# Kernel optimization log

Measured on AMD Instinct MI355X. Metric: run time of the kernel, lower is better.

The kernel has to match this reference:

```python
import jax, jax.numpy as jnp
import numpy as np

EPS = 1e-08


def _norm(H, add):
    # Faithful to GTN.norm: transpose, mask/set diagonal, row-normalize by degree, transpose back.
    # The original O(N^3) mm(deg_inv_diag, H) is expressed as an O(N^2) row scaling (same math).
    Ht = H.T
    n = Ht.shape[0]
    eye = jnp.eye(n, dtype=H.dtype)
    Ht = Ht * (1.0 - eye)
    if add:
        Ht = Ht + eye
    deg = jnp.sum(Ht, axis=1)
    deg_inv = jnp.where(deg == 0, 0.0, 1.0 / (deg + EPS))
    return (deg_inv[:, None] * Ht).T


def _gtconv(A, w):
    # A: [E, N, N]; w: [C, E, 1, 1] -> softmax over E, weighted sum of adjacency channels.
    s = jax.nn.softmax(w[:, :, 0, 0], axis=1)  # [C, E]
    return jnp.einsum('ce,eij->cij', s, A)     # [C, N, N]


def setup_inputs() -> dict:
    key = jax.random.key(0)
    k = jax.random.split(key, 6)
    E, N, C, w_in, w_out = 5, 2048, 2, 256, 64
    A = jax.random.uniform(k[0], (E, N, N), dtype=jnp.float32)
    X = jax.random.normal(k[1], (N, w_in), dtype=jnp.float32)
    conv_w_l0_1 = jax.random.normal(k[2], (C, E, 1, 1), dtype=jnp.float32)
    conv_w_l0_2 = jax.random.normal(k[3], (C, E, 1, 1), dtype=jnp.float32)
    conv_w_l1 = jax.random.normal(k[4], (C, E, 1, 1), dtype=jnp.float32)
    gcn_weight = jax.random.normal(k[5], (w_in, w_out), dtype=jnp.float32) * (1.0 / np.sqrt(w_in))
    return {"A": A, "X": X, "conv_w_l0_1": conv_w_l0_1, "conv_w_l0_2": conv_w_l0_2,
            "conv_w_l1": conv_w_l1, "gcn_weight": gcn_weight}


def reference(A, X, conv_w_l0_1, conv_w_l0_2, conv_w_l1, gcn_weight):
    N = A.shape[1]
    # Layer 0 (first=True): two GTConvs, meta-path composition via bmm.
    a = _gtconv(A, conv_w_l0_1)            # [C, N, N]
    b = _gtconv(A, conv_w_l0_2)            # [C, N, N]
    H = jnp.einsum('cij,cjk->cik', a, b)   # [C, N, N]
    # Layer 1 (first=False): normalize per channel, then compose with new conv.
    H = jax.vmap(lambda h: _norm(h, False))(H)
    a1 = _gtconv(A, conv_w_l1)
    H = jnp.einsum('cij,cjk->cik', H, a1)
    # GCN readout per channel: mm(norm_add(H_c).T, X @ W), relu, concat along features.
    Xw = X @ gcn_weight                     # [N, w_out]
    Hn = jax.vmap(lambda h: _norm(h, True))(H)   # [C, N, N]
    Xc = jax.nn.relu(jnp.einsum('cji,jk->cik', Hn, Xw))  # [C, N, w_out]
    X_ = jnp.transpose(Xc, (1, 0, 2)).reshape(N, -1)     # [N, C*w_out]
    return X_
```

## Files before the change

kernel.cpp:

```cpp
#include <hip/hip_runtime.h>
#include <cstdint>
#include <cstddef>

typedef unsigned short u16;
typedef __attribute__((ext_vector_type(8))) short short8;
typedef __attribute__((ext_vector_type(4))) float v4f;

static constexpr size_t NN = (size_t)2048 * 2048;
#define N2 2048

typedef __attribute__((address_space(1))) const unsigned int guint;
typedef __attribute__((address_space(3))) unsigned int luint;

__device__ __forceinline__ float b2f_bits(uint32_t hi) { union { uint32_t u; float f; } v; v.u = hi; return v.f; }
__device__ __forceinline__ float b2f(u16 x) { return b2f_bits((uint32_t)x << 16); }
__device__ __forceinline__ u16 f2b(float f) {
  union { float f; uint32_t u; } v; v.f = f;
  uint32_t r = v.u + 0x7fffu + ((v.u >> 16) & 1u);
  return (u16)(r >> 16);
}
__device__ __forceinline__ uint2 pack4(const float* f) {
  uint2 u;
  u.x = (uint32_t)f2b(f[0]) | ((uint32_t)f2b(f[1]) << 16);
  u.y = (uint32_t)f2b(f[2]) | ((uint32_t)f2b(f[3]) << 16);
  return u;
}
__device__ __forceinline__ uint4 pack8(const float* f) {
  uint4 u;
  u.x = (uint32_t)f2b(f[0]) | ((uint32_t)f2b(f[1]) << 16);
  u.y = (uint32_t)f2b(f[2]) | ((uint32_t)f2b(f[3]) << 16);
  u.z = (uint32_t)f2b(f[4]) | ((uint32_t)f2b(f[5]) << 16);
  u.w = (uint32_t)f2b(f[6]) | ((uint32_t)f2b(f[7]) << 16);
  return u;
}

__global__ __launch_bounds__(256, 6) void conv_kernel(
    const float* __restrict__ A, const float* __restrict__ w1,
    const float* __restrict__ w2, const float* __restrict__ w3,
    const float* __restrict__ X, const float* __restrict__ W,
    u16* __restrict__ abf, u16* __restrict__ bbt, u16* __restrict__ a1t,
    u16* __restrict__ Xwt)
{
  __shared__ float lb[32][33];
  __shared__ float la[32][33];
  const int t = threadIdx.x;
  const int i0 = blockIdx.y * 32, j0 = blockIdx.x * 32;

  float s1[2][5], s2[2][5], s3[2][5];
  {
    const float* wsrc[3] = { w1, w2, w3 };
    float (*sdst[3])[5] = { s1, s2, s3 };
    for (int q = 0; q < 3; ++q)
      for (int c = 0; c < 2; ++c) {
        float v[5], m = -1e30f, sum = 0.f;
        for (int e = 0; e < 5; ++e) { v[e] = wsrc[q][c * 5 + e]; m = fmaxf(m, v[e]); }
        for (int e = 0; e < 5; ++e) { v[e] = expf(v[e] - m); sum += v[e]; }
        for (int e = 0; e < 5; ++e) sdst[q][c][e] = v[e] / sum;
      }
  }

  const int row = t >> 3;
  const int c4 = (t & 7) * 4;
  float cst[2][4];

  {
    float fa[5][4];
    for (int e = 0; e < 5; ++e) {
      float4 v = *(const float4*)(A + (size_t)e * NN + (size_t)(i0 + row) * N2 + (j0 + c4));
      fa[e][0] = v.x; fa[e][1] = v.y; fa[e][2] = v.z; fa[e][3] = v.w;
    }
    for (int c = 0; c < 2; ++c) {
      float av[4] = {0,0,0,0}, bv[4] = {0,0,0,0}, cv[4] = {0,0,0,0};
      for (int e = 0; e < 5; ++e)
        #pragma unroll
        for (int u = 0; u < 4; ++u) {
          av[u] += s1[c][e] * fa[e][u];
          bv[u] += s2[c][e] * fa[e][u];
          cv[u] += s3[c][e] * fa[e][u];
        }
      *(uint2*)(abf + (size_t)c * NN + (size_t)(i0 + row) * N2 + (j0 + c4)) = pack4(av);
      float* ldst = (c == 0) ? &lb[row][c4] : &la[row][c4];
      #pragma unroll
      for (int u = 0; u < 4; ++u) ldst[u] = bv[u];
      #pragma unroll
      for (int u = 0; u < 4; ++u) cst[c][u] = cv[u];
    }
  }
  __syncthreads();
  {
    float t0[4], t1[4];
    #pragma unroll
    for (int u = 0; u < 4; ++u) { t0[u] = lb[c4 + u][row]; t1[u] = la[c4 + u][row]; }
    *(uint2*)(bbt + 0 * NN + (size_t)(j0 + row) * N2 + (i0 + c4)) = pack4(t0);
    *(uint2*)(bbt + 1 * NN + (size_t)(j0 + row) * N2 + (i0 + c4)) = pack4(t1);
  }
  __syncthreads();
  #pragma unroll
  for (int u = 0; u < 4; ++u) { lb[row][c4 + u] = cst[0][u]; la[row][c4 + u] = cst[1][u]; }
  __syncthreads();
  {
    float t0[4], t1[4];
    #pragma unroll
    for (int u = 0; u < 4; ++u) { t0[u] = lb[c4 + u][row]; t1[u] = la[c4 + u][row]; }
    *(uint2*)(a1t + 0 * NN + (size_t)(j0 + row) * N2 + (i0 + c4)) = pack4(t0);
    *(uint2*)(a1t + 1 * NN + (size_t)(j0 + row) * N2 + (i0 + c4)) = pack4(t1);
  }
  if (blockIdx.y < 8) {
    const int n = (int)(blockIdx.y * 64 + blockIdx.x) * 4 + (t >> 6);
    const int k = t & 63;
    float acc = 0.f;
    for (int m = 0; m < 256; ++m)
      acc += X[n * 256 + m] * W[m * 64 + k];
    Xwt[(size_t)k * N2 + n] = f2b(acc);
  }
}

template<bool TOUT>
__global__ __launch_bounds__(256, 5) void gemm_kernel(
    const u16* __restrict__ Ain, const u16* __restrict__ Btin,
    u16* __restrict__ Cout, float* __restrict__ csp, float* __restrict__ diag)
{
  const int c = blockIdx.z;
  const u16* Ac = Ain + (size_t)c * NN;
  const u16* Bc = Btin + (size_t)c * NN;
  const int m0 = blockIdx.y * 128, n0 = blockIdx.x * 64;
  const int t = threadIdx.x, w = t >> 6, lane = t & 63;
  const int quad = lane >> 4, r = lane & 15;
  __shared__ u16 SM[128 * 64 + 64 * 64];
  u16* As = SM;
  u16* Bs = SM + 128 * 64;

  v4f zero4 = { 0.f, 0.f, 0.f, 0.f };
  v4f acc[2][4];
  #pragma unroll
  for (int i = 0; i < 2; ++i)
    #pragma unroll
    for (int j = 0; j < 4; ++j) acc[i][j] = zero4;

  const int srow = lane >> 3;
  const int sgran = (lane & 7) ^ srow;

  for (int kt = 0; kt < 2048; kt += 64) {
    __syncthreads();
    #pragma unroll
    for (int i = 0; i < 4; ++i) {
      const int chunk = i * 4 + w;
      const u16* ga = Ac + (size_t)(m0 + chunk * 8 + srow) * N2 + kt + sgran * 8;
      __builtin_amdgcn_global_load_lds((guint*)ga, (luint*)(As + chunk * 512), 16, 0, 0);
    }
    #pragma unroll
    for (int i = 0; i < 2; ++i) {
      const int chunk = i * 4 + w;
      const u16* gb = Bc + (size_t)(n0 + chunk * 8 + srow) * N2 + kt + sgran * 8;
      __builtin_amdgcn_global_load_lds((guint*)gb, (luint*)(Bs + chunk * 512), 16, 0, 0);
    }
    __syncthreads();
    #pragma unroll
    for (int ks = 0; ks < 2; ++ks) {
      const int sl = ((ks * 4 + quad) ^ (r & 7)) * 8;
      short8 af[2], bf[4];
      #pragma unroll
      for (int i = 0; i < 2; ++i)
        af[i] = *(const short8*)(As + (w * 32 + i * 16 + r) * 64 + sl);
      #pragma unroll
      for (int j = 0; j < 4; ++j)
        bf[j] = *(const short8*)(Bs + (j * 16 + r) * 64 + sl);
      #pragma unroll
      for (int i = 0; i < 2; ++i)
        #pragma unroll
        for (int j = 0; j < 4; ++j)
          acc[i][j] = __builtin_amdgcn_mfma_f32_16x16x32_bf16(af[i], bf[j], acc[i][j], 0, 0, 0);
    }
  }
  if ((int)(blockIdx.x >> 1) == (int)blockIdx.y) {
    #pragma unroll
    for (int i = 0; i < 2; ++i) {
      const int rowg = m0 + w * 32 + i * 16 + quad * 4;
      #pragma unroll
      for (int j = 0; j < 4; ++j) {
        const int colg = n0 + j * 16 + r;
        #pragma unroll
        for (int g = 0; g < 4; ++g)
          if (rowg + g == colg) diag[c * N2 + colg] = acc[i][j][g];
      }
    }
  }
  if constexpr (!TOUT) {
    u16* Cc = Cout + (size_t)c * NN;
    #pragma unroll
    for (int i = 0; i < 2; ++i) {
      const int rowg = m0 + w * 32 + i * 16 + quad * 4;
      #pragma unroll
      for (int j = 0; j < 4; ++j) {
        const int colg = n0 + j * 16 + r;
        #pragma unroll
        for (int g = 0; g < 4; ++g)
          Cc[(size_t)(rowg + g) * N2 + colg] = f2b(acc[i][j][g]);
      }
    }
  }
  float s[4];
  #pragma unroll
  for (int j = 0; j < 4; ++j) {
    s[j] = 0.f;
    #pragma unroll
    for (int i = 0; i < 2; ++i)
      #pragma unroll
      for (int g = 0; g < 4; ++g) s[j] += acc[i][j][g];
    s[j] += __shfl_xor(s[j], 16);
    s[j] += __shfl_xor(s[j], 32);
  }
  __syncthreads();
  float* csl = (float*)SM;
  if (quad == 0) {
    #pragma unroll
    for (int j = 0; j < 4; ++j) csl[w * 64 + j * 16 + r] = s[j];
  }
  __syncthreads();
  if (t < 64) {
    const float v = csl[t] + csl[64 + t] + csl[128 + t] + csl[192 + t];
    csp[((size_t)(c * 16) + blockIdx.y) * N2 + n0 + t] = v;
  }
  if constexpr (TOUT) {
    __syncthreads();
    u16* tb = SM;
    #pragma unroll
    for (int i = 0; i < 2; ++i) {
      #pragma unroll
      for (int j = 0; j < 4; ++j) {
        #pragma unroll
        for (int g = 0; g < 4; ++g)
          tb[(j * 16 + r) * 136 + (w * 32 + i * 16 + quad * 4 + g)] = f2b(acc[i][j][g]);
      }
    }
    __syncthreads();
    u16* Cc = Cout + (size_t)c * NN;
    const int rown = t >> 2, seg = t & 3;
    const u16* ps = tb + rown * 136 + seg * 32;
    uint4* pd = (uint4*)(Cc + (size_t)(n0 + rown) * N2 + m0 + seg * 32);
    pd[0] = ((const uint4*)ps)[0];
    pd[1] = ((const uint4*)ps)[1];
    pd[2] = ((const uint4*)ps)[2];
    pd[3] = ((const uint4*)ps)[3];
  }
}

__global__ void colinv_kernel(const float* __restrict__ csp, const float* __restrict__ diag, float* __restrict__ ci)
{
  const int idx = blockIdx.x * 256 + threadIdx.x;
  float cs = 0.f;
  const int c = idx >> 11, q = idx & 2047;
  #pragma unroll
  for (int s = 0; s < 16; ++s) cs += csp[((size_t)(c * 16) + s) * N2 + q];
  const float deg = cs - diag[idx];
  ci[idx] = (deg == 0.f) ? 0.f : 1.f / (deg + 1e-8f);
}

__global__ __launch_bounds__(256) void scale_kernel(const u16* __restrict__ H, const float* __restrict__ ci, u16* __restrict__ Hn)
{
  const int idx = blockIdx.x * 256 + threadIdx.x;
  const int q0 = (idx & 255) * 8;
  const int p = (idx >> 8) & 2047;
  const int c = idx >> 19;
  const u16* src = H + (size_t)c * NN + (size_t)p * N2 + q0;
  const float* cv = ci + c * N2 + q0;
  uint4 hu = *(const uint4*)src;
  float h[8];
  h[0] = b2f_bits(hu.x << 16); h[1] = b2f_bits(hu.x & 0xffff0000u);
  h[2] = b2f_bits(hu.y << 16); h[3] = b2f_bits(hu.y & 0xffff0000u);
  h[4] = b2f_bits(hu.z << 16); h[5] = b2f_bits(hu.z & 0xffff0000u);
  h[6] = b2f_bits(hu.w << 16); h[7] = b2f_bits(hu.w & 0xffff0000u);
  float f[8];
  #pragma unroll
  for (int u = 0; u < 8; ++u) {
    float v = h[u] * cv[u];
    f[u] = (q0 + u == p) ? 0.f : v;
  }
  *(uint4*)(Hn + (size_t)c * NN + (size_t)p * N2 + q0) = pack8(f);
}

__global__ __launch_bounds__(256) void tgemm_kernel(
    const u16* __restrict__ H2t, const u16* __restrict__ Xwt, float* __restrict__ Tp)
{
  const int c = blockIdx.z, split = blockIdx.y;
  const int m0 = blockIdx.x * 128;
  const u16* Ac = H2t + (size_t)c * NN;
  const int t = threadIdx.x, w = t >> 6, lane = t & 63;
  const int quad = lane >> 4, r = lane & 15;
  __shared__ u16 As[128 * 64];
  __shared__ u16 Bs[64 * 64];

  v4f zero4 = { 0.f, 0.f, 0.f, 0.f };
  v4f acc[2][4];
  #pragma unroll
  for (int i = 0; i < 2; ++i)
    #pragma unroll
    for (int j = 0; j < 4; ++j) acc[i][j] = zero4;

  const int srow = lane >> 3;
  const int sgran = (lane & 7) ^ srow;

  for (int kk = 0; kk < 2; ++kk) {
    const int kt = split * 128 + kk * 64;
    __syncthreads();
    #pragma unroll
    for (int i = 0; i < 4; ++i) {
      const int chunk = i * 4 + w;
      const u16* ga = Ac + (size_t)(m0 + chunk * 8 + srow) * N2 + kt + sgran * 8;
      __builtin_amdgcn_global_load_lds((guint*)ga, (luint*)(As + chunk * 512), 16, 0, 0);
    }
    #pragma unroll
    for (int i = 0; i < 2; ++i) {
      const int chunk = i * 4 + w;
      const u16* gb = Xwt + (size_t)(chunk * 8 + srow) * N2 + kt + sgran * 8;
      __builtin_amdgcn_global_load_lds((guint*)gb, (luint*)(Bs + chunk * 512), 16, 0, 0);
    }
    __syncthreads();
    #pragma unroll
    for (int ks = 0; ks < 2; ++ks) {
      const int sl = ((ks * 4 + quad) ^ (r & 7)) * 8;
      short8 af[2], bf[4];
      #pragma unroll
      for (int i = 0; i < 2; ++i)
        af[i] = *(const short8*)(As + (w * 32 + i * 16 + r) * 64 + sl);
      #pragma unroll
      for (int j = 0; j < 4; ++j)
        bf[j] = *(const short8*)(Bs + (j * 16 + r) * 64 + sl);
      #pragma unroll
      for (int i = 0; i < 2; ++i)
        #pragma unroll
        for (int j = 0; j < 4; ++j)
          acc[i][j] = __builtin_amdgcn_mfma_f32_16x16x32_bf16(af[i], bf[j], acc[i][j], 0, 0, 0);
    }
  }
  const size_t pbase = (size_t)(split * 2 + c) * 2048;
  #pragma unroll
  for (int i = 0; i < 2; ++i) {
    const int rowg = m0 + w * 32 + i * 16 + quad * 4;
    #pragma unroll
    for (int j = 0; j < 4; ++j) {
      const int colg = j * 16 + r;
      #pragma unroll
      for (int g = 0; g < 4; ++g)
        Tp[(pbase + rowg + g) * 64 + colg] = acc[i][j][g];
    }
  }
}

__global__ void epilogue_kernel(const float* __restrict__ Tp, const float* __restrict__ cspb,
                                const float* __restrict__ diag2, const u16* __restrict__ Xwt,
                                float* __restrict__ out)
{
  const int idx = blockIdx.x * 256 + threadIdx.x;
  const int k = idx & 63;
  const int c = (idx >> 6) & 1;
  const int i = idx >> 7;
  float T = 0.f, cs = 0.f;
  #pragma unroll
  for (int s = 0; s < 16; ++s) {
    T  += Tp[((size_t)(s * 2 + c) * 2048 + i) * 64 + k];
    cs += cspb[((size_t)(c * 16) + s) * N2 + i];
  }
  const float hd = diag2[c * N2 + i];
  const float xw = b2f(Xwt[(size_t)k * N2 + i]);
  const float deg = cs - hd + 1.0f;
  const float dinv = (deg == 0.f) ? 0.f : 1.f / (deg + 1e-8f);
  float v = dinv * (T - hd * xw + xw);
  v = v > 0.f ? v : 0.f;
  out[(size_t)i * 128 + c * 64 + k] = v;
}

extern "C" void kernel_launch(void* const* d_in, const int* in_sizes, int n_in,
                              void* d_out, int out_size, void* d_ws, size_t ws_size,
                              hipStream_t stream) {
  const float* A  = (const float*)d_in[0];
  const float* X  = (const float*)d_in[1];
  const float* w1 = (const float*)d_in[2];
  const float* w2 = (const float*)d_in[3];
  const float* w3 = (const float*)d_in[4];
  const float* W  = (const float*)d_in[5];
  float* out = (float*)d_out;
  char* ws = (char*)d_ws;

  u16*   abf   = (u16*)(ws + 0);
  u16*   bbt   = (u16*)(ws + 16777216);
  u16*   a1t   = (u16*)(ws + 33554432);
  u16*   Hbf   = (u16*)(ws + 50331648);
  u16*   Hn    = (u16*)(ws + 67108864);
  u16*   Xwt   = (u16*)(ws + 83886080);
  float* cspa  = (float*)(ws + 84148224);
  float* cspb  = (float*)(ws + 84410368);
  float* diag1 = (float*)(ws + 84672512);
  float* diag2 = (float*)(ws + 84688896);
  float* ci1   = (float*)(ws + 84705280);
  u16*   H2t   = (u16*)(ws + 0);
  float* Tp    = (float*)(ws + 16777216);

  conv_kernel<<<dim3(64, 64), 256, 0, stream>>>(A, w1, w2, w3, X, W, abf, bbt, a1t, Xwt);
  gemm_kernel<false><<<dim3(32, 16, 2), 256, 0, stream>>>(abf, bbt, Hbf, cspa, diag1);
  colinv_kernel<<<16, 256, 0, stream>>>(cspa, diag1, ci1);
  scale_kernel<<<4096, 256, 0, stream>>>(Hbf, ci1, Hn);
  gemm_kernel<true><<<dim3(32, 16, 2), 256, 0, stream>>>(Hn, a1t, H2t, cspb, diag2);
  tgemm_kernel<<<dim3(16, 16, 2), 256, 0, stream>>>(H2t, Xwt, Tp);
  epilogue_kernel<<<1024, 256, 0, stream>>>(Tp, cspb, diag2, Xwt, out);
}
```

Measured before the change: 267.3 us.

## Reassociate second N×N GEMM into skinny GEMMs against Xw

Result: slower. 285.4 us (+6.8%).

```diff
diff --git a/kernel.cpp b/kernel.cpp
--- a/kernel.cpp
+++ b/kernel.cpp
@@ -25,13 +25,11 @@
   u.y = (uint32_t)f2b(f[2]) | ((uint32_t)f2b(f[3]) << 16);
   return u;
 }
-__device__ __forceinline__ uint4 pack8(const float* f) {
-  uint4 u;
-  u.x = (uint32_t)f2b(f[0]) | ((uint32_t)f2b(f[1]) << 16);
-  u.y = (uint32_t)f2b(f[2]) | ((uint32_t)f2b(f[3]) << 16);
-  u.z = (uint32_t)f2b(f[4]) | ((uint32_t)f2b(f[5]) << 16);
-  u.w = (uint32_t)f2b(f[6]) | ((uint32_t)f2b(f[7]) << 16);
-  return u;
+__device__ __forceinline__ void unp8(uint4 u, float* f) {
+  f[0] = b2f_bits(u.x << 16); f[1] = b2f_bits(u.x & 0xffff0000u);
+  f[2] = b2f_bits(u.y << 16); f[3] = b2f_bits(u.y & 0xffff0000u);
+  f[4] = b2f_bits(u.z << 16); f[5] = b2f_bits(u.z & 0xffff0000u);
+  f[6] = b2f_bits(u.w << 16); f[7] = b2f_bits(u.w & 0xffff0000u);
 }
 
 __global__ __launch_bounds__(256, 6) void conv_kernel(
@@ -39,7 +37,7 @@
     const float* __restrict__ w2, const float* __restrict__ w3,
     const float* __restrict__ X, const float* __restrict__ W,
     u16* __restrict__ abf, u16* __restrict__ bbt, u16* __restrict__ a1t,
-    u16* __restrict__ Xwt)
+    u16* __restrict__ a1r, u16* __restrict__ Xwt)
 {
   __shared__ float lb[32][33];
   __shared__ float la[32][33];
@@ -79,6 +77,7 @@
           cv[u] += s3[c][e] * fa[e][u];
         }
       *(uint2*)(abf + (size_t)c * NN + (size_t)(i0 + row) * N2 + (j0 + c4)) = pack4(av);
+      *(uint2*)(a1r + (size_t)c * NN + (size_t)(i0 + row) * N2 + (j0 + c4)) = pack4(cv);
       float* ldst = (c == 0) ? &lb[row][c4] : &la[row][c4];
       #pragma unroll
       for (int u = 0; u < 4; ++u) ldst[u] = bv[u];
@@ -245,46 +244,12 @@
   }
 }
 
-__global__ void colinv_kernel(const float* __restrict__ csp, const float* __restrict__ diag, float* __restrict__ ci)
-{
-  const int idx = blockIdx.x * 256 + threadIdx.x;
-  float cs = 0.f;
-  const int c = idx >> 11, q = idx & 2047;
-  #pragma unroll
-  for (int s = 0; s < 16; ++s) cs += csp[((size_t)(c * 16) + s) * N2 + q];
-  const float deg = cs - diag[idx];
-  ci[idx] = (deg == 0.f) ? 0.f : 1.f / (deg + 1e-8f);
-}
-
-__global__ __launch_bounds__(256) void scale_kernel(const u16* __restrict__ H, const float* __restrict__ ci, u16* __restrict__ Hn)
-{
-  const int idx = blockIdx.x * 256 + threadIdx.x;
-  const int q0 = (idx & 255) * 8;
-  const int p = (idx >> 8) & 2047;
-  const int c = idx >> 19;
-  const u16* src = H + (size_t)c * NN + (size_t)p * N2 + q0;
-  const float* cv = ci + c * N2 + q0;
-  uint4 hu = *(const uint4*)src;
-  float h[8];
-  h[0] = b2f_bits(hu.x << 16); h[1] = b2f_bits(hu.x & 0xffff0000u);
-  h[2] = b2f_bits(hu.y << 16); h[3] = b2f_bits(hu.y & 0xffff0000u);
-  h[4] = b2f_bits(hu.z << 16); h[5] = b2f_bits(hu.z & 0xffff0000u);
-  h[6] = b2f_bits(hu.w << 16); h[7] = b2f_bits(hu.w & 0xffff0000u);
-  float f[8];
-  #pragma unroll
-  for (int u = 0; u < 8; ++u) {
-    float v = h[u] * cv[u];
-    f[u] = (q0 + u == p) ? 0.f : v;
-  }
-  *(uint4*)(Hn + (size_t)c * NN + (size_t)p * N2 + q0) = pack8(f);
-}
-
-__global__ __launch_bounds__(256) void tgemm_kernel(
-    const u16* __restrict__ H2t, const u16* __restrict__ Xwt, float* __restrict__ Tp)
+__global__ __launch_bounds__(256) void zgemm_kernel(
+    const u16* __restrict__ Ht, const u16* __restrict__ Xwt, float* __restrict__ Zp)
 {
   const int c = blockIdx.z, split = blockIdx.y;
   const int m0 = blockIdx.x * 128;
-  const u16* Ac = H2t + (size_t)c * NN;
+  const u16* Ac = Ht + (size_t)c * NN;
   const int t = threadIdx.x, w = t >> 6, lane = t & 63;
   const int quad = lane >> 4, r = lane & 15;
   __shared__ u16 As[128 * 64];
@@ -333,13 +298,161 @@
           acc[i][j] = __builtin_amdgcn_mfma_f32_16x16x32_bf16(af[i], bf[j], acc[i][j], 0, 0, 0);
     }
   }
-  const size_t pbase = (size_t)(split * 2 + c) * 2048;
+  const size_t pbase = (size_t)(split * 2 + c) * 64;
   #pragma unroll
   for (int i = 0; i < 2; ++i) {
     const int rowg = m0 + w * 32 + i * 16 + quad * 4;
     #pragma unroll
     for (int j = 0; j < 4; ++j) {
       const int colg = j * 16 + r;
+      *(v4f*)(Zp + (pbase + colg) * (size_t)N2 + rowg) = acc[i][j];
+    }
+  }
+}
+
+__global__ void colinv_kernel(const float* __restrict__ csp, const float* __restrict__ diag,
+                              float* __restrict__ ci, float* __restrict__ wv)
+{
+  const int idx = blockIdx.x * 256 + threadIdx.x;
+  float cs = 0.f;
+  const int c = idx >> 11, q = idx & 2047;
+  #pragma unroll
+  for (int s = 0; s < 16; ++s) cs += csp[((size_t)(c * 16) + s) * N2 + q];
+  const float deg = cs - diag[idx];
+  const float v = (deg == 0.f) ? 0.f : 1.f / (deg + 1e-8f);
+  ci[idx] = v;
+  wv[idx] = v * deg;
+}
+
+__global__ __launch_bounds__(256) void dcol_kernel(
+    const u16* __restrict__ Ht, const u16* __restrict__ a1r,
+    const float* __restrict__ ci, const float* __restrict__ wv,
+    float* __restrict__ dp, float* __restrict__ cp)
+{
+  const int qg = blockIdx.x, c = blockIdx.y;
+  const int p0 = threadIdx.x * 8;
+  float dacc[8] = {0,0,0,0,0,0,0,0};
+  float cacc[8] = {0,0,0,0,0,0,0,0};
+  const u16* hb = Ht  + (size_t)c * NN + (size_t)(qg * 16) * N2 + p0;
+  const u16* ab = a1r + (size_t)c * NN + (size_t)(qg * 16) * N2 + p0;
+  for (int qq = 0; qq < 16; ++qq) {
+    const int q = qg * 16 + qq;
+    const float cq = ci[c * N2 + q];
+    const float wq = wv[c * N2 + q];
+    uint4 hu = *(const uint4*)(hb + (size_t)qq * N2);
+    uint4 au = *(const uint4*)(ab + (size_t)qq * N2);
+    float h[8], a[8];
+    unp8(hu, h); unp8(au, a);
+    #pragma unroll
+    for (int u = 0; u < 8; ++u) {
+      cacc[u] += wq * a[u];
+      const float tv = cq * h[u] * a[u];
+      dacc[u] += (p0 + u == q) ? 0.f : tv;
+    }
+  }
+  float* dd = dp + (size_t)(c * 128 + qg) * N2 + p0;
+  float* cd = cp + (size_t)(c * 128 + qg) * N2 + p0;
+  v4f d0 = { dacc[0], dacc[1], dacc[2], dacc[3] };
+  v4f d1 = { dacc[4], dacc[5], dacc[6], dacc[7] };
+  v4f c0 = { cacc[0], cacc[1], cacc[2], cacc[3] };
+  v4f c1 = { cacc[4], cacc[5], cacc[6], cacc[7] };
+  *(v4f*)dd = d0; *(v4f*)(dd + 4) = d1;
+  *(v4f*)cd = c0; *(v4f*)(cd + 4) = c1;
+}
+
+__global__ __launch_bounds__(256) void yfix_kernel(
+    const float* __restrict__ Zp, const float* __restrict__ ci,
+    const float* __restrict__ diag1, const u16* __restrict__ Xwt,
+    u16* __restrict__ Yt)
+{
+  const int idx = blockIdx.x * 256 + threadIdx.x;
+  const int i = idx & 2047, k = (idx >> 11) & 63, c = idx >> 17;
+  float z = 0.f;
+  #pragma unroll
+  for (int s = 0; s < 16; ++s)
+    z += Zp[(size_t)((s * 2 + c) * 64 + k) * N2 + i];
+  const float xw = b2f(Xwt[(size_t)k * N2 + i]);
+  const float y = ci[c * N2 + i] * (z - diag1[c * N2 + i] * xw);
+  Yt[(size_t)c * 64 * N2 + (size_t)k * N2 + i] = f2b(y);
+}
+
+__global__ void fin_kernel(const float* __restrict__ dp, const float* __restrict__ cp,
+                           float* __restrict__ diag2, float* __restrict__ dinv2)
+{
+  const int idx = blockIdx.x * 256 + threadIdx.x;
+  const int c = idx >> 11, i = idx & 2047;
+  float ds = 0.f, cs = 0.f;
+  for (int b = 0; b < 128; ++b) {
+    ds += dp[(size_t)(c * 128 + b) * N2 + i];
+    cs += cp[(size_t)(c * 128 + b) * N2 + i];
+  }
+  const float deg = cs - ds + 1.0f;
+  diag2[idx] = ds;
+  dinv2[idx] = (deg == 0.f) ? 0.f : 1.f / (deg + 1e-8f);
+}
+
+__global__ __launch_bounds__(256) void tgemm_kernel(
+    const u16* __restrict__ a1t, const u16* __restrict__ Yt, float* __restrict__ Tp)
+{
+  const int c = blockIdx.z, split = blockIdx.y;
+  const int m0 = blockIdx.x * 128;
+  const u16* Ac = a1t + (size_t)c * NN;
+  const u16* Bc = Yt + (size_t)c * (64 * (size_t)N2);
+  const int t = threadIdx.x, w = t >> 6, lane = t & 63;
+  const int quad = lane >> 4, r = lane & 15;
+  __shared__ u16 As[128 * 64];
+  __shared__ u16 Bs[64 * 64];
+
+  v4f zero4 = { 0.f, 0.f, 0.f, 0.f };
+  v4f acc[2][4];
+  #pragma unroll
+  for (int i = 0; i < 2; ++i)
+    #pragma unroll
+    for (int j = 0; j < 4; ++j) acc[i][j] = zero4;
+
+  const int srow = lane >> 3;
+  const int sgran = (lane & 7) ^ srow;
+
+  for (int kk = 0; kk < 2; ++kk) {
+    const int kt = split * 128 + kk * 64;
+    __syncthreads();
+    #pragma unroll
+    for (int i = 0; i < 4; ++i) {
+      const int chunk = i * 4 + w;
+      const u16* ga = Ac + (size_t)(m0 + chunk * 8 + srow) * N2 + kt + sgran * 8;
+      __builtin_amdgcn_global_load_lds((guint*)ga, (luint*)(As + chunk * 512), 16, 0, 0);
+    }
+    #pragma unroll
+    for (int i = 0; i < 2; ++i) {
+      const int chunk = i * 4 + w;
+      const u16* gb = Bc + (size_t)(chunk * 8 + srow) * N2 + kt + sgran * 8;
+      __builtin_amdgcn_global_load_lds((guint*)gb, (luint*)(Bs + chunk * 512), 16, 0, 0);
+    }
+    __syncthreads();
+    #pragma unroll
+    for (int ks = 0; ks < 2; ++ks) {
+      const int sl = ((ks * 4 + quad) ^ (r & 7)) * 8;
+      short8 af[2], bf[4];
+      #pragma unroll
+      for (int i = 0; i < 2; ++i)
+        af[i] = *(const short8*)(As + (w * 32 + i * 16 + r) * 64 + sl);
+      #pragma unroll
+      for (int j = 0; j < 4; ++j)
+        bf[j] = *(const short8*)(Bs + (j * 16 + r) * 64 + sl);
+      #pragma unroll
+      for (int i = 0; i < 2; ++i)
+        #pragma unroll
+        for (int j = 0; j < 4; ++j)
+          acc[i][j] = __builtin_amdgcn_mfma_f32_16x16x32_bf16(af[i], bf[j], acc[i][j], 0, 0, 0);
+    }
+  }
+  const size_t pbase = (size_t)(split * 2 + c) * 2048;
+  #pragma unroll
+  for (int i = 0; i < 2; ++i) {
+    const int rowg = m0 + w * 32 + i * 16 + quad * 4;
+    #pragma unroll
+    for (int j = 0; j < 4; ++j) {
+      const int colg = j * 16 + r;
       #pragma unroll
       for (int g = 0; g < 4; ++g)
         Tp[(pbase + rowg + g) * 64 + colg] = acc[i][j][g];
@@ -347,25 +460,22 @@
   }
 }
 
-__global__ void epilogue_kernel(const float* __restrict__ Tp, const float* __restrict__ cspb,
-                                const float* __restrict__ diag2, const u16* __restrict__ Xwt,
+__global__ void epilogue_kernel(const float* __restrict__ Tp, const float* __restrict__ diag2,
+                                const float* __restrict__ dinv2, const u16* __restrict__ Xwt,
                                 float* __restrict__ out)
 {
   const int idx = blockIdx.x * 256 + threadIdx.x;
   const int k = idx & 63;
   const int c = (idx >> 6) & 1;
   const int i = idx >> 7;
-  float T = 0.f, cs = 0.f;
-  #pragma unroll
-  for (int s = 0; s < 16; ++s) {
-    T  += Tp[((size_t)(s * 2 + c) * 2048 + i) * 64 + k];
-    cs += cspb[((size_t)(c * 16) + s) * N2 + i];
-  }
+  float T = 0.f;
+  #pragma unroll
+  for (int s = 0; s < 16; ++s)
+    T += Tp[((size_t)(s * 2 + c) * 2048 + i) * 64 + k];
   const float hd = diag2[c * N2 + i];
+  const float dv = dinv2[c * N2 + i];
   const float xw = b2f(Xwt[(size_t)k * N2 + i]);
-  const float deg = cs - hd + 1.0f;
-  const float dinv = (deg == 0.f) ? 0.f : 1.f / (deg + 1e-8f);
-  float v = dinv * (T - hd * xw + xw);
+  float v = dv * (T - hd * xw + xw);
   v = v > 0.f ? v : 0.f;
   out[(size_t)i * 128 + c * 64 + k] = v;
 }
@@ -385,22 +495,28 @@
   u16*   abf   = (u16*)(ws + 0);
   u16*   bbt   = (u16*)(ws + 16777216);
   u16*   a1t   = (u16*)(ws + 33554432);
-  u16*   Hbf   = (u16*)(ws + 50331648);
-  u16*   Hn    = (u16*)(ws + 67108864);
+  u16*   a1r   = (u16*)(ws + 50331648);
+  u16*   Ht    = (u16*)(ws + 67108864);
   u16*   Xwt   = (u16*)(ws + 83886080);
   float* cspa  = (float*)(ws + 84148224);
-  float* cspb  = (float*)(ws + 84410368);
-  float* diag1 = (float*)(ws + 84672512);
-  float* diag2 = (float*)(ws + 84688896);
-  float* ci1   = (float*)(ws + 84705280);
-  u16*   H2t   = (u16*)(ws + 0);
-  float* Tp    = (float*)(ws + 16777216);
-
-  conv_kernel<<<dim3(64, 64), 256, 0, stream>>>(A, w1, w2, w3, X, W, abf, bbt, a1t, Xwt);
-  gemm_kernel<false><<<dim3(32, 16, 2), 256, 0, stream>>>(abf, bbt, Hbf, cspa, diag1);
-  colinv_kernel<<<16, 256, 0, stream>>>(cspa, diag1, ci1);
-  scale_kernel<<<4096, 256, 0, stream>>>(Hbf, ci1, Hn);
-  gemm_kernel<true><<<dim3(32, 16, 2), 256, 0, stream>>>(Hn, a1t, H2t, cspb, diag2);
-  tgemm_kernel<<<dim3(16, 16, 2), 256, 0, stream>>>(H2t, Xwt, Tp);
-  epilogue_kernel<<<1024, 256, 0, stream>>>(Tp, cspb, diag2, Xwt, out);
-}
+  float* diag1 = (float*)(ws + 84410368);
+  float* ci1   = (float*)(ws + 84426752);
+  float* w2v   = (float*)(ws + 84443136);
+  float* diag2 = (float*)(ws + 84459520);
+  float* dinv2 = (float*)(ws + 84475904);
+  float* Zp    = (float*)(ws + 0);
+  float* dp    = (float*)(ws + 16777216);
+  float* cp    = (float*)(ws + 18874368);
+  u16*   Yt    = (u16*)(ws + 20971520);
+  float* Tp    = (float*)(ws + 50331648);
+
+  conv_kernel<<<dim3(64, 64), 256, 0, stream>>>(A, w1, w2, w3, X, W, abf, bbt, a1t, a1r, Xwt);
+  gemm_kernel<true><<<dim3(32, 16, 2), 256, 0, stream>>>(abf, bbt, Ht, cspa, diag1);
+  zgemm_kernel<<<dim3(16, 16, 2), 256, 0, stream>>>(Ht, Xwt, Zp);
+  colinv_kernel<<<16, 256, 0, stream>>>(cspa, diag1, ci1, w2v);
+  dcol_kernel<<<dim3(128, 2), 256, 0, stream>>>(Ht, a1r, ci1, w2v, dp, cp);
+  yfix_kernel<<<1024, 256, 0, stream>>>(Zp, ci1, diag1, Xwt, Yt);
+  fin_kernel<<<16, 256, 0, stream>>>(dp, cp, diag2, dinv2);
+  tgemm_kernel<<<dim3(16, 16, 2), 256, 0, stream>>>(a1t, Yt, Tp);
+  epilogue_kernel<<<1024, 256, 0, stream>>>(Tp, diag2, dinv2, Xwt, out);
+}
```
